# Performance work log

Hardware: AMD Instinct MI355X
Metric: run time of the kernel (lower is better)

Reference implementation:

```python
import jax, jax.numpy as jnp
import numpy as np

K0 = 16
TAU = -2.053748910631823
EPS = 1e-06


def setup_inputs() -> dict:
    key = jax.random.key(0)
    k1, k2, k3 = jax.random.split(key, 3)
    B, DIN, DOUT = 32768, 1024, 1024
    x = jax.random.normal(k1, (B, DIN), dtype=jnp.float32)
    weight = jax.random.normal(k2, (DOUT, DIN), dtype=jnp.float32) * 0.02
    bias = jax.random.normal(k3, (DOUT,), dtype=jnp.float32) * 0.02
    return {"x": x, "weight": weight, "bias": bias}


def reference(x, weight, bias):
    # Kernel loads x and w as fp16 and accumulates in fp32.
    x16 = x.astype(jnp.float16)        # [B, DIN]
    w16 = weight.astype(jnp.float16)   # [DOUT, DIN]

    xa, wa = x16[:, :K0], w16[:, :K0]
    # Warmup partial dot product over the first K0 columns: y1[b,n] = sum_k x[b,k]*w[n,k]
    y1 = jnp.einsum("bk,nk->bn", xa, wa, preferred_element_type=jnp.float32)
    # s2[b,n] = sum_k (x[b,k]*w[n,k])^2 = sum_k x^2 * w^2
    s2 = jnp.einsum("bk,nk->bn", xa * xa, wa * wa, preferred_element_type=jnp.float32)

    denom = jnp.sqrt(s2 / (K0 + EPS) + EPS)
    tstat = jnp.abs(y1) / jnp.maximum(denom, EPS)
    passed = tstat < TAU                     # early-terminate mask (true => skip remaining cols)
    still_active = ~passed                   # [B, DOUT]

    # Remaining columns contribute only where still_active.
    rest = jnp.einsum("bk,nk->bn", x16[:, K0:], w16[:, K0:], preferred_element_type=jnp.float32)
    acc = y1 + rest * still_active.astype(jnp.float32)

    out = acc + bias.astype(jnp.float32)
    return out.astype(x.dtype)
```

## Files before the change

### kernel.cpp

```cpp
#include <hip/hip_runtime.h>

typedef _Float16 f16;
typedef f16 f16x2 __attribute__((ext_vector_type(2)));
typedef f16 f16x4 __attribute__((ext_vector_type(4)));
typedef f16 f16x8 __attribute__((ext_vector_type(8)));
typedef float f32x4 __attribute__((ext_vector_type(4)));

constexpr int Mdim = 32768, Ndim = 1024, Kdim = 1024;
constexpr int BM = 256, BN = 256, BK = 64;
constexpr int NT = Kdim / BK;

static __device__ inline f16x2 cvt2(float a, float b) {
    return __builtin_bit_cast(f16x2, __builtin_amdgcn_cvt_pkrtz(a, b));
}
static __device__ inline f16x4 cvt4(float4 v) {
    f16x2 lo = cvt2(v.x, v.y), hi = cvt2(v.z, v.w);
    return __builtin_shufflevector(lo, hi, 0, 1, 2, 3);
}
static __device__ inline void bar() {
    asm volatile("" ::: "memory");
    __builtin_amdgcn_s_barrier();
    asm volatile("" ::: "memory");
}
static __device__ inline void lgkm0() {
    asm volatile("s_waitcnt lgkmcnt(0)" ::: "memory");
}

__global__ __launch_bounds__(512, 2)
void etrow_gemm(const float* __restrict__ X, const float* __restrict__ W,
                const float* __restrict__ bias, float* __restrict__ out)
{
    __shared__ f16 As[2][BM * BK];
    __shared__ f16 Bs[2][BN * BK];

    const int bid = blockIdx.x;
    const int cpx = gridDim.x >> 3;
    const int wg  = (bid & 7) * cpx + (bid >> 3);
    const int mIdx = wg >> 2;
    const int nIdx = wg & 3;

    const int tid  = threadIdx.x;
    const int lane = tid & 63;
    const int wave = tid >> 6;
    const int wr   = (wave >> 2) * 128;
    const int wc   = (wave & 3) * 64;

    const int r0 = tid >> 4;
    const int c4 = tid & 15;

    const float* xthr = X + (size_t)mIdx * BM * Kdim + r0 * Kdim + c4 * 4;
    const float* wthr = W + (size_t)nIdx * BN * Kdim + r0 * Kdim + c4 * 4;
    const int wbyte = (r0 * 128 + c4 * 8) ^ ((r0 & 7) << 4);
    const int abyte = ((wr + (lane & 15)) * 128 + (lane >> 4) * 16) ^ ((lane & 7) << 4);
    const int bbyte = ((wc + (lane & 15)) * 128 + (lane >> 4) * 16) ^ ((lane & 7) << 4);
    char* const Ab = (char*)&As[0][0];
    char* const Bb = (char*)&Bs[0][0];

    float4 SA[8], SB[8];
    f32x4 acc[8][4] = {};

    auto issueA = [&](int kt) {
        const float* p = xthr + kt * BK;
        #pragma unroll
        for (int q = 0; q < 8; ++q)
            SA[q] = *(const float4*)(p + q * 32 * Kdim);
    };
    auto issueB = [&](int kt) {
        const float* p = wthr + kt * BK;
        #pragma unroll
        for (int q = 0; q < 8; ++q)
            SB[q] = *(const float4*)(p + q * 32 * Kdim);
    };
    auto cvtWrA = [&](int bufoff) {
        #pragma unroll
        for (int q = 0; q < 8; ++q)
            *(f16x4*)(Ab + bufoff + wbyte + q * 4096) = cvt4(SA[q]);
    };
    auto cvtWrB = [&](int bufoff) {
        #pragma unroll
        for (int q = 0; q < 8; ++q)
            *(f16x4*)(Bb + bufoff + wbyte + q * 4096) = cvt4(SB[q]);
    };

    auto phase = [&](int co, int p) {
        f16x8 af[4], bf[4];
        #pragma unroll
        for (int mi = 0; mi < 4; ++mi)
            af[mi] = *(const f16x8*)(Ab + co + ((abyte + (p * 4 + mi) * 2048)));
        #pragma unroll
        for (int j = 0; j < 4; ++j)
            bf[j] = *(const f16x8*)(Bb + co + ((bbyte + j * 2048)));
        bar();
        lgkm0();
        __builtin_amdgcn_s_setprio(1);
        #pragma unroll
        for (int mi = 0; mi < 4; ++mi)
            #pragma unroll
            for (int j = 0; j < 4; ++j)
                acc[p * 4 + mi][j] = __builtin_amdgcn_mfma_f32_16x16x32_f16(
                    af[mi], bf[j], acc[p * 4 + mi][j], 0, 0, 0);
        #pragma unroll
        for (int mi = 0; mi < 4; ++mi)
            af[mi] = *(const f16x8*)(Ab + co + ((abyte + (p * 4 + mi) * 2048) ^ 64));
        #pragma unroll
        for (int j = 0; j < 4; ++j)
            bf[j] = *(const f16x8*)(Bb + co + ((bbyte + j * 2048) ^ 64));
        #pragma unroll
        for (int mi = 0; mi < 4; ++mi)
            #pragma unroll
            for (int j = 0; j < 4; ++j)
                acc[p * 4 + mi][j] = __builtin_amdgcn_mfma_f32_16x16x32_f16(
                    af[mi], bf[j], acc[p * 4 + mi][j], 0, 0, 0);
        __builtin_amdgcn_s_setprio(0);
        bar();
    };

    issueA(0); cvtWrA(0);
    issueB(0); cvtWrB(0);
    issueA(1); issueB(1);
    lgkm0();
    bar();

    for (int t = 0; t < NT; ++t) {
        const int co = (t & 1) << 15;
        const int no = co ^ 32768;
        const bool h1 = t + 1 < NT, h2 = t + 2 < NT;

        if (h1) cvtWrA(no);
        if (h2) issueA(t + 2);
        phase(co, 0);
        if (h1) cvtWrB(no);
        if (h2) issueB(t + 2);
        phase(co, 1);
    }

    const int col0  = nIdx * BN + wc + (lane & 15);
    const int rbase = mIdx * BM + wr + (lane >> 4) * 4;
    float bv[4];
    #pragma unroll
    for (int n = 0; n < 4; ++n) bv[n] = bias[col0 + n * 16];

    #pragma unroll
    for (int m = 0; m < 8; ++m) {
        #pragma unroll
        for (int j = 0; j < 4; ++j) {
            const int row = rbase + m * 16 + j;
            float* o = out + (size_t)row * Ndim + col0;
            #pragma unroll
            for (int n = 0; n < 4; ++n)
                o[n * 16] = acc[m][n][j] + bv[n];
        }
    }
}

extern "C" void kernel_launch(void* const* d_in, const int* in_sizes, int n_in,
                              void* d_out, int out_size, void* d_ws, size_t ws_size,
                              hipStream_t stream) {
    const float* X  = (const float*)d_in[0];
    const float* W  = (const float*)d_in[1];
    const float* bs = (const float*)d_in[2];
    float* out = (float*)d_out;
    const int grid = (Mdim / BM) * (Ndim / BN);
    etrow_gemm<<<grid, 512, 0, stream>>>(X, W, bs, out);
}
```

Before: 109.0 us.

## Split each K-tile into four quadrant phases with finer interleaved LDS writes

Reorganizes the main loop from two phases per K-tile into four quadrant phases (M-half by N-half). The fp32-to-fp16 LDS writes and global prefetches are split into halves and interleaved between quadrants. A fragments are now loaded one at a time just before use, and B fragments per N-half. The goal is a steadier interleaving of LDS traffic, global loads and MFMA work, with lower register pressure. In exchange it doubles the barriers per tile and re-reads B fragments for the second M-half.

Result: slower. 116.2 us (+6.6%).

```diff
diff --git a/kernel.cpp b/kernel.cpp
--- a/kernel.cpp
+++ b/kernel.cpp
@@ -50,74 +50,67 @@
 
     const float* xthr = X + (size_t)mIdx * BM * Kdim + r0 * Kdim + c4 * 4;
     const float* wthr = W + (size_t)nIdx * BN * Kdim + r0 * Kdim + c4 * 4;
-    const int wbyte = (r0 * 128 + c4 * 8) ^ ((r0 & 7) << 4);
-    const int abyte = ((wr + (lane & 15)) * 128 + (lane >> 4) * 16) ^ ((lane & 7) << 4);
-    const int bbyte = ((wc + (lane & 15)) * 128 + (lane >> 4) * 16) ^ ((lane & 7) << 4);
+    const int wby = (r0 * 128 + c4 * 8) ^ ((r0 & 7) << 4);
+    const int slot  = ((lane >> 4) * 16) ^ ((lane & 7) << 4);
+    const int abyte = (wr + (lane & 15)) * 128 + slot;
+    const int bbyte = (wc + (lane & 15)) * 128 + slot;
     char* const Ab = (char*)&As[0][0];
     char* const Bb = (char*)&Bs[0][0];
 
-    float4 SA[8], SB[8];
+    float4 SX[8], SW[8];
     f32x4 acc[8][4] = {};
 
-    auto issueA = [&](int kt) {
+    auto issueX = [&](int kt) {
         const float* p = xthr + kt * BK;
         #pragma unroll
         for (int q = 0; q < 8; ++q)
-            SA[q] = *(const float4*)(p + q * 32 * Kdim);
+            SX[q] = *(const float4*)(p + (size_t)q * 32 * Kdim);
     };
-    auto issueB = [&](int kt) {
+    auto issueW = [&](int kt) {
         const float* p = wthr + kt * BK;
         #pragma unroll
         for (int q = 0; q < 8; ++q)
-            SB[q] = *(const float4*)(p + q * 32 * Kdim);
+            SW[q] = *(const float4*)(p + (size_t)q * 32 * Kdim);
     };
-    auto cvtWrA = [&](int bufoff) {
+    auto cvtWrX = [&](int off, int half) {
         #pragma unroll
-        for (int q = 0; q < 8; ++q)
-            *(f16x4*)(Ab + bufoff + wbyte + q * 4096) = cvt4(SA[q]);
+        for (int q = half * 4; q < half * 4 + 4; ++q)
+            *(f16x4*)(Ab + off + wby + q * 4096) = cvt4(SX[q]);
     };
-    auto cvtWrB = [&](int bufoff) {
+    auto cvtWrW = [&](int off, int half) {
         #pragma unroll
-        for (int q = 0; q < 8; ++q)
-            *(f16x4*)(Bb + bufoff + wbyte + q * 4096) = cvt4(SB[q]);
+        for (int q = half * 4; q < half * 4 + 4; ++q)
+            *(f16x4*)(Bb + off + wby + q * 4096) = cvt4(SW[q]);
     };
 
-    auto phase = [&](int co, int p) {
-        f16x8 af[4], bf[4];
+    f16x8 bf[2][2];
+    auto bfRead = [&](int co, int nh) {
         #pragma unroll
-        for (int mi = 0; mi < 4; ++mi)
-            af[mi] = *(const f16x8*)(Ab + co + ((abyte + (p * 4 + mi) * 2048)));
+        for (int s = 0; s < 2; ++s)
+            #pragma unroll
+            for (int n = 0; n < 2; ++n)
+                bf[s][n] = *(const f16x8*)
+                    (Bb + co + ((bbyte + (nh * 2 + n) * 2048) ^ (s << 6)));
+    };
+    auto quad = [&](int co, int mh, int nh) {
         #pragma unroll
-        for (int j = 0; j < 4; ++j)
-            bf[j] = *(const f16x8*)(Bb + co + ((bbyte + j * 2048)));
-        bar();
-        lgkm0();
-        __builtin_amdgcn_s_setprio(1);
-        #pragma unroll
-        for (int mi = 0; mi < 4; ++mi)
+        for (int s = 0; s < 2; ++s)
             #pragma unroll
-            for (int j = 0; j < 4; ++j)
-                acc[p * 4 + mi][j] = __builtin_amdgcn_mfma_f32_16x16x32_f16(
-                    af[mi], bf[j], acc[p * 4 + mi][j], 0, 0, 0);
-        #pragma unroll
-        for (int mi = 0; mi < 4; ++mi)
-            af[mi] = *(const f16x8*)(Ab + co + ((abyte + (p * 4 + mi) * 2048) ^ 64));
-        #pragma unroll
-        for (int j = 0; j < 4; ++j)
-            bf[j] = *(const f16x8*)(Bb + co + ((bbyte + j * 2048) ^ 64));
-        #pragma unroll
-        for (int mi = 0; mi < 4; ++mi)
-            #pragma unroll
-            for (int j = 0; j < 4; ++j)
-                acc[p * 4 + mi][j] = __builtin_amdgcn_mfma_f32_16x16x32_f16(
-                    af[mi], bf[j], acc[p * 4 + mi][j], 0, 0, 0);
-        __builtin_amdgcn_s_setprio(0);
-        bar();
+            for (int m = 0; m < 4; ++m) {
+                f16x8 af = *(const f16x8*)
+                    (Ab + co + ((abyte + (mh * 4 + m) * 2048) ^ (s << 6)));
+                #pragma unroll
+                for (int n = 0; n < 2; ++n)
+                    acc[mh * 4 + m][nh * 2 + n] =
+                        __builtin_amdgcn_mfma_f32_16x16x32_f16(
+                            af, bf[s][n], acc[mh * 4 + m][nh * 2 + n], 0, 0, 0);
+            }
     };
 
-    issueA(0); cvtWrA(0);
-    issueB(0); cvtWrB(0);
-    issueA(1); issueB(1);
+    issueX(0); issueW(0);
+    cvtWrX(0, 0); cvtWrX(0, 1);
+    cvtWrW(0, 0); cvtWrW(0, 1);
+    issueX(1); issueW(1);
     lgkm0();
     bar();
 
@@ -126,12 +119,29 @@
         const int no = co ^ 32768;
         const bool h1 = t + 1 < NT, h2 = t + 2 < NT;
 
-        if (h1) cvtWrA(no);
-        if (h2) issueA(t + 2);
-        phase(co, 0);
-        if (h1) cvtWrB(no);
-        if (h2) issueB(t + 2);
-        phase(co, 1);
+        if (h1) cvtWrX(no, 0);
+        bfRead(co, 0);
+        bar(); lgkm0();
+        __builtin_amdgcn_s_setprio(1); quad(co, 0, 0); __builtin_amdgcn_s_setprio(0);
+        bar();
+        if (h1) cvtWrX(no, 1);
+        if (h2) issueX(t + 2);
+        bfRead(co, 1);
+        bar(); lgkm0();
+        __builtin_amdgcn_s_setprio(1); quad(co, 0, 1); __builtin_amdgcn_s_setprio(0);
+        bar();
+        if (h1) cvtWrW(no, 0);
+        bfRead(co, 0);
+        bar(); lgkm0();
+        __builtin_amdgcn_s_setprio(1); quad(co, 1, 0); __builtin_amdgcn_s_setprio(0);
+        bar();
+        if (h1) cvtWrW(no, 1);
+        if (h2) issueW(t + 2);
+        bfRead(co, 1);
+        bar(); lgkm0();
+        __builtin_amdgcn_s_setprio(1); quad(co, 1, 1); __builtin_amdgcn_s_setprio(0);
+        lgkm0();
+        bar();
     }
 
     const int col0  = nIdx * BN + wc + (lane & 15);
```
